# Kernel tuning notes

Measured on AMD Instinct MI355X. Metric: run time of the kernel, lower is better.

Reference implementation:

```python
import jax, jax.numpy as jnp
import numpy as np

N_NODES = 50000
N_EDGES = 800000
D = 128


def setup_inputs() -> dict:
    key = jax.random.key(0)
    ks = jax.random.split(key, 6)
    stdv = 1.0 / np.sqrt(D)
    inputs = {
        "input": jax.random.normal(ks[0], (N_NODES, D), dtype=jnp.float32),
        "h0": jax.random.normal(ks[1], (N_NODES, D), dtype=jnp.float32),
        # COO representation of the (normalized) sparse adjacency
        "vals": jax.random.uniform(ks[2], (N_EDGES,), dtype=jnp.float32) / 16.0,
        "weight": jax.random.uniform(ks[3], (D, D), dtype=jnp.float32, minval=-stdv, maxval=stdv),
        "lamda": jnp.float32(0.5),
        "alpha": jnp.float32(0.1),
        "row": jax.random.randint(ks[4], (N_EDGES,), 0, N_NODES),
        "col": jax.random.randint(ks[5], (N_EDGES,), 0, N_NODES),
        "l": 4,
    }
    return inputs


def reference(input, h0, vals, weight, lamda, alpha, row, col, l):
    # theta = log(lamda / l + 1)
    theta = jnp.log(lamda / l + 1.0)
    # hi = spmm(adj, input): gather source-node features, scale by edge
    # values, scatter-add into destination rows.  [E, D] -> [N, D]
    hi = jax.ops.segment_sum(vals[:, None] * input[col], row, num_segments=input.shape[0])
    # variant=False path
    support = (1.0 - alpha) * hi + alpha * h0
    r = support
    # output = theta * support @ W + (1 - theta) * r
    output = theta * jnp.matmul(support, weight) + (1.0 - theta) * r
    return output
```

## Files before the change

### kernel.cpp

```cpp
#include <hip/hip_runtime.h>
#include <cmath>

constexpr int N_NODES = 50000;
constexpr int N_EDGES = 800000;
constexpr int D = 128;
constexpr int CAP = 32;
constexpr int OVF_CAP = 8192;

constexpr int NBIN = 256;
constexpr int RPP  = 196;
constexpr int QCAP = 4096;
constexpr int QCNT_STRIDE = 16;
constexpr int EPB_BIN = 4096;
constexpr int BIN_BLOCKS = (N_EDGES + EPB_BIN - 1) / EPB_BIN;
constexpr int CAST_BLOCKS = (N_NODES * D / 8 + 255) / 256;

constexpr size_t OFF_OVFCNT = 16384;
constexpr size_t OFF_QUEUE  = 16448;
constexpr size_t OFF_CNT    = 8405056;
constexpr size_t OFF_BUCKET = 8605056;
constexpr size_t OFF_OVF    = 15005056;
constexpr size_t OFF_PACKED = 15136128;
constexpr size_t OFF_WT     = 27936128;

typedef __attribute__((ext_vector_type(8))) short bf16x8;
typedef __attribute__((ext_vector_type(4))) float f32x4;

__device__ __forceinline__ unsigned bf16rn(float f) {
    unsigned u = __float_as_uint(f);
    return (u + 0x7fffu + ((u >> 16) & 1u)) >> 16;
}
__device__ __forceinline__ float bf_lo(unsigned u) { return __uint_as_float(u << 16); }
__device__ __forceinline__ float bf_hi(unsigned u) { return __uint_as_float(u & 0xffff0000u); }

__device__ __forceinline__ unsigned enc_val(float v) {
    int m = (int)(v * 1048576.0f + 0.5f);
    if (m > 65535) m = 65535;
    if (m < 0) m = 0;
    return (unsigned)m;
}

__global__ __launch_bounds__(256) void binsort_cast(
    const int* __restrict__ row, const int* __restrict__ col,
    const float* __restrict__ vals, const float* __restrict__ input,
    const float* __restrict__ weight,
    int* __restrict__ qcnt, uint2* __restrict__ queue,
    int* __restrict__ ovf_cnt, int4* __restrict__ ovf,
    unsigned* __restrict__ packed, ushort* __restrict__ wt)
{
    const int tid = threadIdx.x;
    if (blockIdx.x < BIN_BLOCKS) {
        __shared__ uint2 lq[EPB_BIN];
        __shared__ int hist[NBIN], off[NBIN], gbase[NBIN], fill[NBIN];
        __shared__ int wsum[4];

        int er[16]; unsigned ec[16];
        const int gi0 = blockIdx.x * (EPB_BIN / 4);
        #pragma unroll
        for (int it = 0; it < 4; ++it) {
            int gi = gi0 + it * 256 + tid;
            int4 r4 = make_int4(-1, -1, -1, -1);
            int4 c4 = make_int4(0, 0, 0, 0);
            float4 v4 = make_float4(0.f, 0.f, 0.f, 0.f);
            if (gi < N_EDGES / 4) {
                r4 = ((const int4*)row)[gi];
                c4 = ((const int4*)col)[gi];
                v4 = ((const float4*)vals)[gi];
            }
            er[it*4+0] = r4.x; ec[it*4+0] = (unsigned)c4.x | (enc_val(v4.x) << 16);
            er[it*4+1] = r4.y; ec[it*4+1] = (unsigned)c4.y | (enc_val(v4.y) << 16);
            er[it*4+2] = r4.z; ec[it*4+2] = (unsigned)c4.z | (enc_val(v4.z) << 16);
            er[it*4+3] = r4.w; ec[it*4+3] = (unsigned)c4.w | (enc_val(v4.w) << 16);
        }
        hist[tid] = 0;
        __syncthreads();
        #pragma unroll
        for (int j = 0; j < 16; ++j)
            if (er[j] >= 0) atomicAdd(&hist[er[j] / RPP], 1);
        __syncthreads();
        int h = hist[tid];
        int v = h;
        #pragma unroll
        for (int s = 1; s < 64; s <<= 1) {
            int t = __shfl_up(v, s, 64);
            if ((tid & 63) >= s) v += t;
        }
        if ((tid & 63) == 63) wsum[tid >> 6] = v;
        __syncthreads();
        int w = tid >> 6, woff = 0;
        if (w > 0) woff += wsum[0];
        if (w > 1) woff += wsum[1];
        if (w > 2) woff += wsum[2];
        off[tid]   = woff + v - h;
        gbase[tid] = atomicAdd(&qcnt[tid * QCNT_STRIDE], h);
        fill[tid]  = 0;
        __syncthreads();
        #pragma unroll
        for (int j = 0; j < 16; ++j)
            if (er[j] >= 0) {
                int b = er[j] / RPP;
                int p = atomicAdd(&fill[b], 1);
                lq[off[b] + p] = make_uint2(ec[j], (unsigned)er[j]);
            }
        __syncthreads();
        const int total = off[NBIN - 1] + hist[NBIN - 1];
        for (int i = tid; i < total; i += 256) {
            uint2 e = lq[i];
            int r = (int)e.y;
            int b = r / RPP;
            int dst = gbase[b] + (i - off[b]);
            if (dst < QCAP) queue[(size_t)b * QCAP + dst] = e;
            else {
                int o = atomicAdd(ovf_cnt, 1);
                if (o < OVF_CAP) ovf[o] = make_int4(r, (int)(e.x & 0xffffu),
                    __float_as_int((float)(e.x >> 16) * (1.0f / 1048576.0f)), 0);
            }
        }
    } else if (blockIdx.x < BIN_BLOCKS + CAST_BLOCKS) {
        int i = (blockIdx.x - BIN_BLOCKS) * 256 + tid;
        if (i >= N_NODES * D / 8) return;
        const float4* f = (const float4*)(input + (size_t)i * 8);
        float4 a = f[0], b = f[1];
        uint4 o;
        o.x = bf16rn(a.x) | (bf16rn(a.y) << 16);
        o.y = bf16rn(a.z) | (bf16rn(a.w) << 16);
        o.z = bf16rn(b.x) | (bf16rn(b.y) << 16);
        o.w = bf16rn(b.z) | (bf16rn(b.w) << 16);
        ((uint4*)packed)[i] = o;
    } else {
        #pragma unroll
        for (int j = 0; j < 64; ++j) {
            int idx = tid + j * 256;
            int k = idx >> 7, n = idx & 127;
            wt[n * 128 + k] = (ushort)bf16rn(weight[idx]);
        }
    }
}

__global__ __launch_bounds__(256) void bucket_build(
    const uint2* __restrict__ queue, const int* __restrict__ qcnt,
    int* __restrict__ ovf_cnt, int4* __restrict__ ovf,
    int* __restrict__ cnt, unsigned* __restrict__ bucket)
{
    __shared__ int cl[RPP];
    __shared__ unsigned lb[RPP * CAP];

    const int b = blockIdx.x;
    const int tid = threadIdx.x;
    if (tid < RPP) cl[tid] = 0;
    __syncthreads();

    int nb = qcnt[b * QCNT_STRIDE];
    if (nb > QCAP) nb = QCAP;
    for (int i = tid; i < nb; i += 256) {
        uint2 e = queue[(size_t)b * QCAP + i];
        int r  = (int)e.y;
        int rl = r - b * RPP;
        int pos = atomicAdd(&cl[rl], 1);
        if (pos < CAP) lb[rl * CAP + pos] = e.x;
        else {
            int o = atomicAdd(ovf_cnt, 1);
            if (o < OVF_CAP) ovf[o] = make_int4(r, (int)(e.x & 0xffffu),
                __float_as_int((float)(e.x >> 16) * (1.0f / 1048576.0f)), 0);
        }
    }
    __syncthreads();

    if (tid < RPP) {
        int r = b * RPP + tid;
        if (r < N_NODES) cnt[r] = cl[tid];
    }
    for (int i = tid; i < RPP * CAP; i += 256) {
        int gidx = b * RPP * CAP + i;
        if (gidx < N_NODES * CAP) bucket[gidx] = lb[i];
    }
}

__global__ __launch_bounds__(256) void gather_support(
    const unsigned* __restrict__ packed,
    const float* __restrict__ h0,
    const float* __restrict__ alpha_p,
    const int* __restrict__ cnt,
    const unsigned* __restrict__ bucket,
    const int* __restrict__ ovf_cnt_p,
    const int4* __restrict__ ovf,
    float* __restrict__ support)
{
    const float alpha = *alpha_p;
    const float oma = 1.0f - alpha;
    const int wv   = threadIdx.x >> 6;
    const int lane = threadIdx.x & 63;
    const int q    = lane & 15;
    const int slot = lane >> 4;

    const int g = blockIdx.x * 4 + wv;
    if (g >= N_NODES) return;

    int n = cnt[g];
    int novf = *ovf_cnt_p;
    if (novf > OVF_CAP) novf = OVF_CAP;
    if (n > CAP) n = CAP;
    const unsigned* b = bucket + (size_t)g * CAP;
    const uint4* pk = (const uint4*)packed;

    const int q4 = (n + 3) >> 2;
    const int s0 = slot * q4;
    int s1 = s0 + q4; if (s1 > n) s1 = n;

    float acc[8] = {0.f, 0.f, 0.f, 0.f, 0.f, 0.f, 0.f, 0.f};
    for (int e = s0; e < s1; e += 4) {
        int rem = s1 - e;
        unsigned m0 = b[e];
        unsigned m1 = (rem > 1) ? b[e + 1] : 0u;
        unsigned m2 = (rem > 2) ? b[e + 2] : 0u;
        unsigned m3 = (rem > 3) ? b[e + 3] : 0u;
        uint4 x0 = pk[(size_t)(m0 & 0xffffu) * 16 + q];
        uint4 x1 = pk[(size_t)(m1 & 0xffffu) * 16 + q];
        uint4 x2 = pk[(size_t)(m2 & 0xffffu) * 16 + q];
        uint4 x3 = pk[(size_t)(m3 & 0xffffu) * 16 + q];
        float v0 = (float)(m0 >> 16) * (1.0f / 1048576.0f);
        float v1 = (float)(m1 >> 16) * (1.0f / 1048576.0f);
        float v2 = (float)(m2 >> 16) * (1.0f / 1048576.0f);
        float v3 = (float)(m3 >> 16) * (1.0f / 1048576.0f);
        acc[0] += v0 * bf_lo(x0.x); acc[1] += v0 * bf_hi(x0.x);
        acc[2] += v0 * bf_lo(x0.y); acc[3] += v0 * bf_hi(x0.y);
        acc[4] += v0 * bf_lo(x0.z); acc[5] += v0 * bf_hi(x0.z);
        acc[6] += v0 * bf_lo(x0.w); acc[7] += v0 * bf_hi(x0.w);
        acc[0] += v1 * bf_lo(x1.x); acc[1] += v1 * bf_hi(x1.x);
        acc[2] += v1 * bf_lo(x1.y); acc[3] += v1 * bf_hi(x1.y);
        acc[4] += v1 * bf_lo(x1.z); acc[5] += v1 * bf_hi(x1.z);
        acc[6] += v1 * bf_lo(x1.w); acc[7] += v1 * bf_hi(x1.w);
        acc[0] += v2 * bf_lo(x2.x); acc[1] += v2 * bf_hi(x2.x);
        acc[2] += v2 * bf_lo(x2.y); acc[3] += v2 * bf_hi(x2.y);
        acc[4] += v2 * bf_lo(x2.z); acc[5] += v2 * bf_hi(x2.z);
        acc[6] += v2 * bf_lo(x2.w); acc[7] += v2 * bf_hi(x2.w);
        acc[0] += v3 * bf_lo(x3.x); acc[1] += v3 * bf_hi(x3.x);
        acc[2] += v3 * bf_lo(x3.y); acc[3] += v3 * bf_hi(x3.y);
        acc[4] += v3 * bf_lo(x3.z); acc[5] += v3 * bf_hi(x3.z);
        acc[6] += v3 * bf_lo(x3.w); acc[7] += v3 * bf_hi(x3.w);
    }
    #pragma unroll
    for (int j = 0; j < 8; ++j) {
        acc[j] += __shfl_xor(acc[j], 16);
        acc[j] += __shfl_xor(acc[j], 32);
    }
    if (slot == 0) {
        for (int o = 0; o < novf; ++o) {
            int4 mm = ovf[o];
            if (mm.x == g) {
                float v = __int_as_float(mm.z);
                uint4 x = pk[(size_t)mm.y * 16 + q];
                acc[0] += v * bf_lo(x.x); acc[1] += v * bf_hi(x.x);
                acc[2] += v * bf_lo(x.y); acc[3] += v * bf_hi(x.y);
                acc[4] += v * bf_lo(x.z); acc[5] += v * bf_hi(x.z);
                acc[6] += v * bf_lo(x.w); acc[7] += v * bf_hi(x.w);
            }
        }
        const float* hp = h0 + (size_t)g * D + q * 8;
        float4 ha = *(const float4*)(hp);
        float4 hb = *(const float4*)(hp + 4);
        float* sp = support + (size_t)g * D + q * 8;
        float4 sa, sb;
        sa.x = oma * acc[0] + alpha * ha.x;
        sa.y = oma * acc[1] + alpha * ha.y;
        sa.z = oma * acc[2] + alpha * ha.z;
        sa.w = oma * acc[3] + alpha * ha.w;
        sb.x = oma * acc[4] + alpha * hb.x;
        sb.y = oma * acc[5] + alpha * hb.y;
        sb.z = oma * acc[6] + alpha * hb.z;
        sb.w = oma * acc[7] + alpha * hb.w;
        *(float4*)(sp) = sa;
        *(float4*)(sp + 4) = sb;
    }
}

__global__ __launch_bounds__(256) void gemm_mfma(
    const ushort* __restrict__ wt,
    const float* __restrict__ lamda_p,
    const int* __restrict__ l_p,
    float* __restrict__ data)
{
    constexpr int SP = 136;
    __shared__ ushort sA[64 * SP];
    __shared__ ushort sB[128 * SP];

    const int tid = threadIdx.x;
    const float lamda = *lamda_p;
    const float theta = logf(lamda / (float)(*l_p) + 1.0f);
    const float omt = 1.0f - theta;
    const int row0 = blockIdx.x * 64;

    #pragma unroll
    for (int j = 0; j < 8; ++j) {
        int idx = j * 256 + tid;
        int n  = idx >> 4;
        int k8 = (idx & 15) << 3;
        *(uint4*)(&sB[n * SP + k8]) = ((const uint4*)wt)[idx];
    }
    #pragma unroll
    for (int j = 0; j < 8; ++j) {
        int idx = j * 256 + tid;
        int rr = idx >> 5;
        int c4 = (idx & 31) << 2;
        int g = row0 + rr;
        float4 s = make_float4(0.f, 0.f, 0.f, 0.f);
        if (g < N_NODES) s = *(const float4*)(data + (size_t)g * D + c4);
        uint2 pkv;
        pkv.x = bf16rn(s.x) | (bf16rn(s.y) << 16);
        pkv.y = bf16rn(s.z) | (bf16rn(s.w) << 16);
        *(uint2*)(&sA[rr * SP + c4]) = pkv;
    }
    __syncthreads();

    const int wave = tid >> 6;
    const int lane = tid & 63;
    const int m    = lane & 15;
    const int quad = lane >> 4;
    const int arow = wave * 16 + m;

    f32x4 acc[8] = {};
    #pragma unroll
    for (int kb = 0; kb < 4; ++kb) {
        bf16x8 a = *(const bf16x8*)(&sA[arow * SP + kb * 32 + quad * 8]);
        #pragma unroll
        for (int nt = 0; nt < 8; ++nt) {
            bf16x8 b = *(const bf16x8*)(&sB[(nt * 16 + m) * SP + kb * 32 + quad * 8]);
            acc[nt] = __builtin_amdgcn_mfma_f32_16x16x32_bf16(a, b, acc[nt], 0, 0, 0);
        }
    }

    const int gbase = row0 + wave * 16 + quad * 4;
    #pragma unroll
    for (int nt = 0; nt < 8; ++nt) {
        int colb = nt * 16 + m;
        #pragma unroll
        for (int i = 0; i < 4; ++i) {
            int g = gbase + i;
            if (g < N_NODES) {
                size_t off = (size_t)g * D + colb;
                float s = data[off];
                data[off] = theta * acc[nt][i] + omt * s;
            }
        }
    }
}

extern "C" void kernel_launch(void* const* d_in, const int* in_sizes, int n_in,
                              void* d_out, int out_size, void* d_ws, size_t ws_size,
                              hipStream_t stream) {
    const float* input  = (const float*)d_in[0];
    const float* h0     = (const float*)d_in[1];
    const float* vals   = (const float*)d_in[2];
    const float* weight = (const float*)d_in[3];
    const float* lamda  = (const float*)d_in[4];
    const float* alpha  = (const float*)d_in[5];
    const int*   row    = (const int*)d_in[6];
    const int*   col    = (const int*)d_in[7];
    const int*   l      = (const int*)d_in[8];
    float* out = (float*)d_out;

    char* ws = (char*)d_ws;
    int*      qcnt    = (int*)ws;
    int*      ovf_cnt = (int*)(ws + OFF_OVFCNT);
    uint2*    queue   = (uint2*)(ws + OFF_QUEUE);
    int*      cnt     = (int*)(ws + OFF_CNT);
    unsigned* bucket  = (unsigned*)(ws + OFF_BUCKET);
    int4*     ovf     = (int4*)(ws + OFF_OVF);
    unsigned* packed  = (unsigned*)(ws + OFF_PACKED);
    ushort*   wt      = (ushort*)(ws + OFF_WT);

    hipMemsetAsync(ws, 0, OFF_QUEUE, stream);

    binsort_cast<<<BIN_BLOCKS + CAST_BLOCKS + 1, 256, 0, stream>>>(
        row, col, vals, input, weight, qcnt, queue, ovf_cnt, ovf, packed, wt);

    bucket_build<<<NBIN, 256, 0, stream>>>(queue, qcnt, ovf_cnt, ovf, cnt, bucket);

    int gatherb = (N_NODES + 3) / 4;
    gather_support<<<gatherb, 256, 0, stream>>>(
        packed, h0, alpha, cnt, bucket, ovf_cnt, ovf, out);

    int gemmb = (N_NODES + 63) / 64;
    gemm_mfma<<<gemmb, 256, 0, stream>>>(wt, lamda, l, out);
}
```

Measured before the change: 192.3 us.

## Fuse binsort, bucket build, gather and GEMM into one cooperative kernel

Replaces the memset plus four separate launches with a single persistent cooperative kernel that uses grid.sync between phases. Binning writes per-block offsets and counts, so no atomics on global counters or memset are needed. The bucket build now does a prefix scan plus binary search to locate queue entries, and the GEMM streams the weight in 32-column chunks to cut shared memory. This removes launch gaps and the memset, but adds grid-wide barriers and limits occupancy to the cooperative grid size. The per-partition overflow is capped at 64 entries, which could drop edges if a partition overflows further.

```diff
diff --git a/kernel.cpp b/kernel.cpp
--- a/kernel.cpp
+++ b/kernel.cpp
@@ -1,20 +1,36 @@
 #include <hip/hip_runtime.h>
+#include <hip/hip_cooperative_groups.h>
 #include <cmath>
+
+namespace cg = cooperative_groups;
 
 constexpr int N_NODES = 50000;
 constexpr int N_EDGES = 800000;
 constexpr int D = 128;
 constexpr int CAP = 32;
 constexpr int OVF_CAP = 8192;
-
+constexpr int POVF_CAP = 64;
 constexpr int NBIN = 256;
 constexpr int RPP  = 196;
+constexpr int SP   = 136;
+
+constexpr int F_EPB = 3072;
+constexpr int F_NB  = (N_EDGES + F_EPB - 1) / F_EPB;
+
+constexpr size_t FO_CNT2   = 267264;
+constexpr size_t FO_QUEUE  = 534528;
+constexpr size_t FO_CNT    = 6948864;
+constexpr size_t FO_POVFC  = 7148864;
+constexpr size_t FO_POVF   = 7149888;
+constexpr size_t FO_BUCKET = 7280960;
+constexpr size_t FO_PACKED = 13680960;
+constexpr size_t FO_WT     = 26480960;
+
 constexpr int QCAP = 4096;
 constexpr int QCNT_STRIDE = 16;
 constexpr int EPB_BIN = 4096;
 constexpr int BIN_BLOCKS = (N_EDGES + EPB_BIN - 1) / EPB_BIN;
 constexpr int CAST_BLOCKS = (N_NODES * D / 8 + 255) / 256;
-
 constexpr size_t OFF_OVFCNT = 16384;
 constexpr size_t OFF_QUEUE  = 16448;
 constexpr size_t OFF_CNT    = 8405056;
@@ -38,6 +54,325 @@
     if (m > 65535) m = 65535;
     if (m < 0) m = 0;
     return (unsigned)m;
+}
+
+struct SmemBin {
+    uint2 lq[F_EPB];
+    int hist[NBIN], off[NBIN], fill[NBIN];
+    int wsum[4];
+};
+struct SmemBuild {
+    unsigned lb[RPP * CAP];
+    int cl[RPP];
+    int lco[F_NB], lcc[F_NB];
+    int s[F_NB + 1];
+    uint2 lpovf[POVF_CAP];
+    int lpc;
+};
+struct SmemGemm {
+    ushort sA[64 * SP];
+    ushort sB[32 * SP];
+};
+
+__global__ __launch_bounds__(256) void fused_all(
+    const int* __restrict__ row, const int* __restrict__ col,
+    const float* __restrict__ vals, const float* __restrict__ input,
+    const float* __restrict__ h0, const float* __restrict__ weight,
+    const float* __restrict__ lamda_p, const float* __restrict__ alpha_p,
+    const int* __restrict__ l_p,
+    int* __restrict__ off2, int* __restrict__ cnt2, uint2* __restrict__ queue2,
+    int* __restrict__ cnt, int* __restrict__ povfc, uint2* __restrict__ povf,
+    unsigned* __restrict__ bucket, unsigned* __restrict__ packed,
+    ushort* __restrict__ wt, float* __restrict__ out)
+{
+    __shared__ __align__(16) char smem[sizeof(SmemBuild)];
+    cg::grid_group grid = cg::this_grid();
+    const int nb  = (int)gridDim.x;
+    const int bid = (int)blockIdx.x;
+    const int tid = (int)threadIdx.x;
+
+    if (bid < F_NB) {
+        SmemBin* sm = (SmemBin*)smem;
+        const int b = bid;
+        int er[12]; unsigned ec[12];
+        const int gi0 = b * (F_EPB / 4);
+        #pragma unroll
+        for (int it = 0; it < 3; ++it) {
+            int gi = gi0 + it * 256 + tid;
+            int4 r4 = make_int4(-1, -1, -1, -1);
+            int4 c4 = make_int4(0, 0, 0, 0);
+            float4 v4 = make_float4(0.f, 0.f, 0.f, 0.f);
+            if (gi < N_EDGES / 4) {
+                r4 = ((const int4*)row)[gi];
+                c4 = ((const int4*)col)[gi];
+                v4 = ((const float4*)vals)[gi];
+            }
+            er[it*4+0] = r4.x; ec[it*4+0] = (unsigned)c4.x | (enc_val(v4.x) << 16);
+            er[it*4+1] = r4.y; ec[it*4+1] = (unsigned)c4.y | (enc_val(v4.y) << 16);
+            er[it*4+2] = r4.z; ec[it*4+2] = (unsigned)c4.z | (enc_val(v4.z) << 16);
+            er[it*4+3] = r4.w; ec[it*4+3] = (unsigned)c4.w | (enc_val(v4.w) << 16);
+        }
+        sm->hist[tid] = 0;
+        __syncthreads();
+        #pragma unroll
+        for (int j = 0; j < 12; ++j)
+            if (er[j] >= 0) atomicAdd(&sm->hist[er[j] / RPP], 1);
+        __syncthreads();
+        int h = sm->hist[tid];
+        int v = h;
+        #pragma unroll
+        for (int s = 1; s < 64; s <<= 1) {
+            int t = __shfl_up(v, s, 64);
+            if ((tid & 63) >= s) v += t;
+        }
+        if ((tid & 63) == 63) sm->wsum[tid >> 6] = v;
+        __syncthreads();
+        int w = tid >> 6, woff = 0;
+        if (w > 0) woff += sm->wsum[0];
+        if (w > 1) woff += sm->wsum[1];
+        if (w > 2) woff += sm->wsum[2];
+        const int off_t = woff + v - h;
+        sm->off[tid]  = off_t;
+        sm->fill[tid] = 0;
+        __syncthreads();
+        #pragma unroll
+        for (int j = 0; j < 12; ++j)
+            if (er[j] >= 0) {
+                int p = er[j] / RPP;
+                int pos = atomicAdd(&sm->fill[p], 1);
+                sm->lq[sm->off[p] + pos] = make_uint2(ec[j], (unsigned)er[j]);
+            }
+        __syncthreads();
+        const int total = sm->off[NBIN - 1] + sm->hist[NBIN - 1];
+        for (int i = tid; i < total; i += 256)
+            queue2[(size_t)b * F_EPB + i] = sm->lq[i];
+        off2[b * NBIN + tid] = off_t;
+        cnt2[b * NBIN + tid] = h;
+    } else {
+        const int cb0 = bid - F_NB;
+        const int ncb = nb - F_NB;
+        for (int i = cb0 * 256 + tid; i < N_NODES * D / 8; i += ncb * 256) {
+            const float4* f = (const float4*)(input + (size_t)i * 8);
+            float4 a = f[0], b2 = f[1];
+            uint4 o;
+            o.x = bf16rn(a.x)  | (bf16rn(a.y)  << 16);
+            o.y = bf16rn(a.z)  | (bf16rn(a.w)  << 16);
+            o.z = bf16rn(b2.x) | (bf16rn(b2.y) << 16);
+            o.w = bf16rn(b2.z) | (bf16rn(b2.w) << 16);
+            ((uint4*)packed)[i] = o;
+        }
+        if (bid == nb - 1) {
+            #pragma unroll
+            for (int j = 0; j < 64; ++j) {
+                int idx = tid + j * 256;
+                int k = idx >> 7, n = idx & 127;
+                wt[n * 128 + k] = (ushort)bf16rn(weight[idx]);
+            }
+        }
+    }
+    grid.sync();
+
+    for (int p = bid; p < NBIN; p += nb) {
+        SmemBuild* sm = (SmemBuild*)smem;
+        if (tid < RPP) sm->cl[tid] = 0;
+        if (tid == 0) sm->lpc = 0;
+        for (int i = tid; i < F_NB; i += 256) {
+            sm->lco[i] = off2[i * NBIN + p];
+            sm->lcc[i] = cnt2[i * NBIN + p];
+        }
+        __syncthreads();
+        if (tid == 0) {
+            int run = 0;
+            for (int b2 = 0; b2 < F_NB; ++b2) { sm->s[b2] = run; run += sm->lcc[b2]; }
+            sm->s[F_NB] = run;
+        }
+        __syncthreads();
+        const int total_p = sm->s[F_NB];
+        for (int idx = tid; idx < total_p; idx += 256) {
+            int lo = 0, hi = F_NB - 1;
+            while (lo < hi) {
+                int mid = (lo + hi + 1) >> 1;
+                if (sm->s[mid] <= idx) lo = mid; else hi = mid - 1;
+            }
+            int i2 = idx - sm->s[lo];
+            uint2 e = queue2[(size_t)lo * F_EPB + sm->lco[lo] + i2];
+            int rl = (int)e.y - p * RPP;
+            int pos = atomicAdd(&sm->cl[rl], 1);
+            if (pos < CAP) sm->lb[rl * CAP + pos] = e.x;
+            else { int o = atomicAdd(&sm->lpc, 1); if (o < POVF_CAP) sm->lpovf[o] = e; }
+        }
+        __syncthreads();
+        if (tid < RPP) {
+            int r = p * RPP + tid;
+            if (r < N_NODES) cnt[r] = sm->cl[tid];
+        }
+        for (int i = tid; i < RPP * CAP; i += 256) {
+            int gidx = p * RPP * CAP + i;
+            if (gidx < N_NODES * CAP) bucket[gidx] = sm->lb[i];
+        }
+        int pc = sm->lpc; if (pc > POVF_CAP) pc = POVF_CAP;
+        if (tid == 0) povfc[p] = pc;
+        if (tid < pc) povf[p * POVF_CAP + tid] = sm->lpovf[tid];
+        __syncthreads();
+    }
+    grid.sync();
+
+    {
+        const float alpha = *alpha_p;
+        const float oma = 1.0f - alpha;
+        const int wv   = tid >> 6;
+        const int lane = tid & 63;
+        const int q    = lane & 15;
+        const int slot = lane >> 4;
+        const uint4* pk = (const uint4*)packed;
+
+        for (int u = bid; u < (N_NODES + 3) / 4; u += nb) {
+            const int g = u * 4 + wv;
+            if (g >= N_NODES) continue;
+            int n = cnt[g];
+            if (n > CAP) n = CAP;
+            const unsigned* bptr = bucket + (size_t)g * CAP;
+            const int q4 = (n + 3) >> 2;
+            const int s0 = slot * q4;
+            int s1 = s0 + q4; if (s1 > n) s1 = n;
+
+            float acc[8] = {0.f, 0.f, 0.f, 0.f, 0.f, 0.f, 0.f, 0.f};
+            for (int e = s0; e < s1; e += 4) {
+                int rem = s1 - e;
+                unsigned m0 = bptr[e];
+                unsigned m1 = (rem > 1) ? bptr[e + 1] : 0u;
+                unsigned m2 = (rem > 2) ? bptr[e + 2] : 0u;
+                unsigned m3 = (rem > 3) ? bptr[e + 3] : 0u;
+                uint4 x0 = pk[(size_t)(m0 & 0xffffu) * 16 + q];
+                uint4 x1 = pk[(size_t)(m1 & 0xffffu) * 16 + q];
+                uint4 x2 = pk[(size_t)(m2 & 0xffffu) * 16 + q];
+                uint4 x3 = pk[(size_t)(m3 & 0xffffu) * 16 + q];
+                float v0 = (float)(m0 >> 16) * (1.0f / 1048576.0f);
+                float v1 = (float)(m1 >> 16) * (1.0f / 1048576.0f);
+                float v2 = (float)(m2 >> 16) * (1.0f / 1048576.0f);
+                float v3 = (float)(m3 >> 16) * (1.0f / 1048576.0f);
+                acc[0] += v0 * bf_lo(x0.x); acc[1] += v0 * bf_hi(x0.x);
+                acc[2] += v0 * bf_lo(x0.y); acc[3] += v0 * bf_hi(x0.y);
+                acc[4] += v0 * bf_lo(x0.z); acc[5] += v0 * bf_hi(x0.z);
+                acc[6] += v0 * bf_lo(x0.w); acc[7] += v0 * bf_hi(x0.w);
+                acc[0] += v1 * bf_lo(x1.x); acc[1] += v1 * bf_hi(x1.x);
+                acc[2] += v1 * bf_lo(x1.y); acc[3] += v1 * bf_hi(x1.y);
+                acc[4] += v1 * bf_lo(x1.z); acc[5] += v1 * bf_hi(x1.z);
+                acc[6] += v1 * bf_lo(x1.w); acc[7] += v1 * bf_hi(x1.w);
+                acc[0] += v2 * bf_lo(x2.x); acc[1] += v2 * bf_hi(x2.x);
+                acc[2] += v2 * bf_lo(x2.y); acc[3] += v2 * bf_hi(x2.y);
+                acc[4] += v2 * bf_lo(x2.z); acc[5] += v2 * bf_hi(x2.z);
+                acc[6] += v2 * bf_lo(x2.w); acc[7] += v2 * bf_hi(x2.w);
+                acc[0] += v3 * bf_lo(x3.x); acc[1] += v3 * bf_hi(x3.x);
+                acc[2] += v3 * bf_lo(x3.y); acc[3] += v3 * bf_hi(x3.y);
+                acc[4] += v3 * bf_lo(x3.z); acc[5] += v3 * bf_hi(x3.z);
+                acc[6] += v3 * bf_lo(x3.w); acc[7] += v3 * bf_hi(x3.w);
+            }
+            #pragma unroll
+            for (int j = 0; j < 8; ++j) {
+                acc[j] += __shfl_xor(acc[j], 16);
+                acc[j] += __shfl_xor(acc[j], 32);
+            }
+            if (slot == 0) {
+                const int p = g / RPP;
+                int pc = povfc[p]; if (pc > POVF_CAP) pc = POVF_CAP;
+                for (int o = 0; o < pc; ++o) {
+                    uint2 mm = povf[p * POVF_CAP + o];
+                    if ((int)mm.y == g) {
+                        float vv = (float)(mm.x >> 16) * (1.0f / 1048576.0f);
+                        uint4 x = pk[(size_t)(mm.x & 0xffffu) * 16 + q];
+                        acc[0] += vv * bf_lo(x.x); acc[1] += vv * bf_hi(x.x);
+                        acc[2] += vv * bf_lo(x.y); acc[3] += vv * bf_hi(x.y);
+                        acc[4] += vv * bf_lo(x.z); acc[5] += vv * bf_hi(x.z);
+                        acc[6] += vv * bf_lo(x.w); acc[7] += vv * bf_hi(x.w);
+                    }
+                }
+                const float* hp = h0 + (size_t)g * D + q * 8;
+                float4 ha = *(const float4*)(hp);
+                float4 hb = *(const float4*)(hp + 4);
+                float* sp = out + (size_t)g * D + q * 8;
+                float4 sa, sb;
+                sa.x = oma * acc[0] + alpha * ha.x;
+                sa.y = oma * acc[1] + alpha * ha.y;
+                sa.z = oma * acc[2] + alpha * ha.z;
+                sa.w = oma * acc[3] + alpha * ha.w;
+                sb.x = oma * acc[4] + alpha * hb.x;
+                sb.y = oma * acc[5] + alpha * hb.y;
+                sb.z = oma * acc[6] + alpha * hb.z;
+                sb.w = oma * acc[7] + alpha * hb.w;
+                *(float4*)(sp) = sa;
+                *(float4*)(sp + 4) = sb;
+            }
+        }
+    }
+    grid.sync();
+
+    {
+        SmemGemm* sg = (SmemGemm*)smem;
+        const float theta = logf((*lamda_p) / (float)(*l_p) + 1.0f);
+        const float omt = 1.0f - theta;
+        const int wave = tid >> 6;
+        const int lane = tid & 63;
+        const int m    = lane & 15;
+        const int quad = lane >> 4;
+        const int arow = wave * 16 + m;
+
+        for (int t = bid; t < (N_NODES + 63) / 64; t += nb) {
+            const int row0 = t * 64;
+            __syncthreads();
+            #pragma unroll
+            for (int j = 0; j < 8; ++j) {
+                int idx = j * 256 + tid;
+                int rr = idx >> 5;
+                int c4 = (idx & 31) << 2;
+                int g = row0 + rr;
+                float4 s = make_float4(0.f, 0.f, 0.f, 0.f);
+                if (g < N_NODES) s = *(const float4*)(out + (size_t)g * D + c4);
+                uint2 pkv;
+                pkv.x = bf16rn(s.x) | (bf16rn(s.y) << 16);
+                pkv.y = bf16rn(s.z) | (bf16rn(s.w) << 16);
+                *(uint2*)(&sg->sA[rr * SP + c4]) = pkv;
+            }
+            f32x4 acc[8] = {};
+            #pragma unroll
+            for (int cb = 0; cb < 4; ++cb) {
+                __syncthreads();
+                #pragma unroll
+                for (int j = 0; j < 2; ++j) {
+                    int idx = j * 256 + tid;
+                    int nr  = idx >> 4;
+                    int k16 = idx & 15;
+                    *(uint4*)(&sg->sB[nr * SP + (k16 << 3)]) =
+                        ((const uint4*)wt)[(cb * 32 + nr) * 16 + k16];
+                }
+                __syncthreads();
+                #pragma unroll
+                for (int kb = 0; kb < 4; ++kb) {
+                    bf16x8 a = *(const bf16x8*)(&sg->sA[arow * SP + kb * 32 + quad * 8]);
+                    #pragma unroll
+                    for (int nt2 = 0; nt2 < 2; ++nt2) {
+                        bf16x8 bb = *(const bf16x8*)(&sg->sB[(nt2 * 16 + m) * SP + kb * 32 + quad * 8]);
+                        acc[cb * 2 + nt2] =
+                            __builtin_amdgcn_mfma_f32_16x16x32_bf16(a, bb, acc[cb * 2 + nt2], 0, 0, 0);
+                    }
+                }
+            }
+            const int gbase = row0 + wave * 16 + quad * 4;
+            #pragma unroll
+            for (int nt = 0; nt < 8; ++nt) {
+                int colb = nt * 16 + m;
+                #pragma unroll
+                for (int i = 0; i < 4; ++i) {
+                    int g = gbase + i;
+                    if (g < N_NODES) {
+                        size_t offo = (size_t)g * D + colb;
+                        float s = out[offo];
+                        out[offo] = theta * acc[nt][i] + omt * s;
+                    }
+                }
+            }
+        }
+    }
 }
 
 __global__ __launch_bounds__(256) void binsort_cast(
@@ -280,7 +615,6 @@
     const int* __restrict__ l_p,
     float* __restrict__ data)
 {
-    constexpr int SP = 136;
     __shared__ ushort sA[64 * SP];
     __shared__ ushort sB[128 * SP];
 
@@ -358,8 +692,49 @@
     const int*   col    = (const int*)d_in[7];
     const int*   l      = (const int*)d_in[8];
     float* out = (float*)d_out;
-
     char* ws = (char*)d_ws;
+
+    static int coop = -1;
+    static int grid = 0;
+    if (coop == -1) {
+        int perCU = 0;
+        hipError_t e1 = hipOccupancyMaxActiveBlocksPerMultiprocessor(
+            &perCU, fused_all, 256, 0);
+        int ncu = 0;
+        hipDeviceProp_t prop{};
+        int dev = 0;
+        hipGetDevice(&dev);
+        if (hipGetDeviceProperties(&prop, dev) == hipSuccess)
+            ncu = prop.multiProcessorCount;
+        grid = perCU * ncu;
+        if (grid > 2048) grid = 2048;
+        coop = (e1 == hipSuccess && grid >= 320) ? 1 : 0;
+    }
+
+    if (coop == 1) {
+        int*      f_off2   = (int*)ws;
+        int*      f_cnt2   = (int*)(ws + FO_CNT2);
+        uint2*    f_queue  = (uint2*)(ws + FO_QUEUE);
+        int*      f_cnt    = (int*)(ws + FO_CNT);
+        int*      f_povfc  = (int*)(ws + FO_POVFC);
+        uint2*    f_povf   = (uint2*)(ws + FO_POVF);
+        unsigned* f_bucket = (unsigned*)(ws + FO_BUCKET);
+        unsigned* f_packed = (unsigned*)(ws + FO_PACKED);
+        ushort*   f_wt     = (ushort*)(ws + FO_WT);
+
+        void* args[] = {
+            (void*)&row, (void*)&col, (void*)&vals, (void*)&input, (void*)&h0,
+            (void*)&weight, (void*)&lamda, (void*)&alpha, (void*)&l,
+            (void*)&f_off2, (void*)&f_cnt2, (void*)&f_queue, (void*)&f_cnt,
+            (void*)&f_povfc, (void*)&f_povf, (void*)&f_bucket, (void*)&f_packed,
+            (void*)&f_wt, (void*)&out };
+
+        hipError_t e = hipLaunchCooperativeKernel(
+            fused_all, dim3(grid), dim3(256), args, 0, stream);
+        if (e == hipSuccess) return;
+        coop = 0;
+    }
+
     int*      qcnt    = (int*)ws;
     int*      ovf_cnt = (int*)(ws + OFF_OVFCNT);
     uint2*    queue   = (uint2*)(ws + OFF_QUEUE);
```

Result: slower. 433.2 us (+125.3%).
